# Optimization experiments

Hardware: AMD Instinct MI355X
Metric: run time of the kernel (lower is better)

Reference implementation:

```python
import jax, jax.numpy as jnp
import numpy as np

C, PE, L, HEADS = 256, 64, 6, 4
N_GRAPHS, S = 2048, 64            # uniform graphs of S nodes -> dense batch is a reshape
N = N_GRAPHS * S                  # 131072 nodes
E = N * 4                         # 524288 edges
BN_EPS = 1e-5


def _bn(h, g, b):
    # BatchNorm1d, training-mode statistics (biased variance), affine
    m = h.mean(0)
    v = h.var(0)
    return (h - m) / jnp.sqrt(v + BN_EPS) * g + b


def setup_inputs() -> dict:
    key = jax.random.key(0)
    ks = iter(jax.random.split(key, 64))
    def rn(shape, scale=0.05):
        return jax.random.normal(next(ks), shape, dtype=jnp.float32) * scale
    x = jax.random.randint(next(ks), (N, 1), 0, 28)
    pe = jax.random.normal(next(ks), (N, 20), dtype=jnp.float32)
    epg = E // N_GRAPHS
    base = (jnp.arange(E) // epg) * S          # edges stay within their graph
    src = base + jax.random.randint(next(ks), (E,), 0, S)
    dst = base + jax.random.randint(next(ks), (E,), 0, S)
    edge_index = jnp.stack([src, dst])
    edge_attr = jax.random.randint(next(ks), (E,), 0, 4)
    batch = jnp.arange(N) // S
    return dict(
        x=x, pe=pe, edge_index=edge_index, edge_attr=edge_attr, batch=batch,
        node_emb=rn((28, C - PE), 1.0), pe_lin_w=rn((20, PE)), pe_lin_b=jnp.zeros(PE),
        pe_norm_g=jnp.ones(20), pe_norm_b=jnp.zeros(20),
        edge_emb=rn((4, C), 1.0),
        conv_w1=rn((L, C, C)), conv_b1=jnp.zeros((L, C)),
        conv_w2=rn((L, C, C)), conv_b2=jnp.zeros((L, C)),
        attn_in_w=rn((L, C, 3 * C)), attn_in_b=jnp.zeros((L, 3 * C)),
        attn_out_w=rn((L, C, C)), attn_out_b=jnp.zeros((L, C)),
        bn1_g=jnp.ones((L, C)), bn1_b=jnp.zeros((L, C)),
        bn2_g=jnp.ones((L, C)), bn2_b=jnp.zeros((L, C)),
        bn3_g=jnp.ones((L, C)), bn3_b=jnp.zeros((L, C)),
        mlp_w1=rn((L, C, 2 * C)), mlp_b1=jnp.zeros((L, 2 * C)),
        mlp_w2=rn((L, 2 * C, C)), mlp_b2=jnp.zeros((L, C)),
        head_w1=rn((C, C // 2)), head_b1=jnp.zeros(C // 2),
        head_w2=rn((C // 2, C // 4)), head_b2=jnp.zeros(C // 4),
        head_w3=rn((C // 4, 1)), head_b3=jnp.zeros(1),
    )


def reference(x, pe, edge_index, edge_attr, batch, node_emb, pe_lin_w, pe_lin_b,
              pe_norm_g, pe_norm_b, edge_emb, conv_w1, conv_b1, conv_w2, conv_b2,
              attn_in_w, attn_in_b, attn_out_w, attn_out_b,
              bn1_g, bn1_b, bn2_g, bn2_b, bn3_g, bn3_b,
              mlp_w1, mlp_b1, mlp_w2, mlp_b2,
              head_w1, head_b1, head_w2, head_b2, head_w3, head_b3):
    x_pe = _bn(pe, pe_norm_g, pe_norm_b)
    h = jnp.concatenate([node_emb[x[:, 0]], x_pe @ pe_lin_w + pe_lin_b], axis=1)  # [N, C]
    ea = edge_emb[edge_attr]                                                      # [E, C]
    src, dst = edge_index[0], edge_index[1]
    d = C // HEADS
    scale = 1.0 / jnp.sqrt(jnp.float32(d))
    for l in range(L):
        # --- local GINEConv: nn((1+eps)*x_i + sum_j relu(x_j + e_ij)), eps=0 ---
        msg = jax.nn.relu(h[src] + ea)                          # gather + add + relu
        aggr = jax.ops.segment_sum(msg, dst, num_segments=N)    # scatter-add
        z = h + aggr
        hl = jax.nn.relu(z @ conv_w1[l] + conv_b1[l]) @ conv_w2[l] + conv_b2[l]
        hl = _bn(hl + h, bn1_g[l], bn1_b[l])                    # residual + norm1
        # --- global multihead attention on dense batch [G, S, C] ---
        hd = h.reshape(N_GRAPHS, S, C)
        qkv = hd @ attn_in_w[l] + attn_in_b[l]
        q, k, v = jnp.split(qkv, 3, axis=-1)
        q = q.reshape(N_GRAPHS, S, HEADS, d).transpose(0, 2, 1, 3)
        k = k.reshape(N_GRAPHS, S, HEADS, d).transpose(0, 2, 1, 3)
        v = v.reshape(N_GRAPHS, S, HEADS, d).transpose(0, 2, 1, 3)
        a = jax.nn.softmax(jnp.einsum('ghqd,ghkd->ghqk', q, k) * scale, axis=-1)
        o = jnp.einsum('ghqk,ghkd->ghqd', a, v).transpose(0, 2, 1, 3).reshape(N_GRAPHS, S, C)
        o = (o @ attn_out_w[l] + attn_out_b[l]).reshape(N, C)
        ha = _bn(o + h, bn2_g[l], bn2_b[l])                     # residual + norm2
        # --- combine + FFN ---
        out = hl + ha
        ff = jax.nn.relu(out @ mlp_w1[l] + mlp_b1[l]) @ mlp_w2[l] + mlp_b2[l]
        h = _bn(out + ff, bn3_g[l], bn3_b[l])                   # residual + norm3
    pooled = jax.ops.segment_sum(h, batch, num_segments=N_GRAPHS)  # global_add_pool -> [G, C]
    t = jax.nn.relu(pooled @ head_w1 + head_b1)
    t = jax.nn.relu(t @ head_w2 + head_b2)
    return t @ head_w3 + head_b3                                   # [G, 1]
```

## Files before the change

kernel.cpp:

```cpp
#include <hip/hip_runtime.h>

#define N_NODES 131072
#define N_EDGES 524288
#define CCH 256
#define N_GRAPHS_ 2048
#define SEQ 64
#define LAYERS 6

typedef unsigned short US;
typedef __attribute__((ext_vector_type(8))) short v8s;
typedef __attribute__((ext_vector_type(8))) unsigned short v8us;
typedef __attribute__((ext_vector_type(4))) float v4f;

__device__ __forceinline__ float b2f(US u) { return __uint_as_float(((unsigned)u) << 16); }
__device__ __forceinline__ US f2b(float f) {
    unsigned u = __float_as_uint(f);
    return (US)((u + 0x7fff + ((u >> 16) & 1)) >> 16);
}
__device__ __forceinline__ void gload16(const US* g, US* l) {
    __builtin_amdgcn_global_load_lds(
        (const __attribute__((address_space(1))) unsigned int*)g,
        (__attribute__((address_space(3))) unsigned int*)l, 16, 0, 0);
}

__device__ float g_stats[512];
__device__ float g_aff1[512];
__device__ float g_aff2[512];
__device__ float g_aff3[512];
__device__ float g_pe[40];
__device__ float g_peaff[40];
__device__ US    g_wt[6 * 655360];
__device__ int   g_csr[N_EDGES];
__device__ int   g_off[N_GRAPHS_ * 65];

__global__ __launch_bounds__(256) void wt_k(const float* __restrict__ cw1, const float* __restrict__ cw2,
                                            const float* __restrict__ aiw, const float* __restrict__ aow,
                                            const float* __restrict__ mw1, const float* __restrict__ mw2) {
    __shared__ float t[64][65];
    int b = blockIdx.x;
    int l = b / 160, r = b % 160;
    const float* src; int ldw, ldk, ctiles; size_t doff;
    if (r < 16)      { src = cw1 + (size_t)l * 65536;  ldw = 256; ldk = 256; ctiles = 4;  doff = 0;      }
    else if (r < 32) { src = cw2 + (size_t)l * 65536;  ldw = 256; ldk = 256; ctiles = 4;  doff = 65536;  r -= 16; }
    else if (r < 80) { src = aiw + (size_t)l * 196608; ldw = 768; ldk = 256; ctiles = 12; doff = 131072; r -= 32; }
    else if (r < 96) { src = aow + (size_t)l * 65536;  ldw = 256; ldk = 256; ctiles = 4;  doff = 327680; r -= 80; }
    else if (r < 128){ src = mw1 + (size_t)l * 131072; ldw = 512; ldk = 256; ctiles = 8;  doff = 393216; r -= 96; }
    else             { src = mw2 + (size_t)l * 131072; ldw = 256; ldk = 512; ctiles = 4;  doff = 524288; r -= 128; }
    int kt = r / ctiles, ct = r % ctiles;
    int k0 = kt * 64, c0 = ct * 64;
    US* dst = g_wt + (size_t)l * 655360 + doff;
    int tid = threadIdx.x;
    int rr = tid >> 4, c4 = (tid & 15) * 4;
    #pragma unroll
    for (int j = 0; j < 4; j++) {
        float4 v = *(const float4*)(src + (size_t)(k0 + rr + j * 16) * ldw + c0 + c4);
        t[rr + j * 16][c4 + 0] = v.x; t[rr + j * 16][c4 + 1] = v.y;
        t[rr + j * 16][c4 + 2] = v.z; t[rr + j * 16][c4 + 3] = v.w;
    }
    __syncthreads();
    #pragma unroll
    for (int j = 0; j < 4; j++) {
        int crow = rr + j * 16;
        ushort4 o;
        o.x = f2b(t[c4 + 0][crow]); o.y = f2b(t[c4 + 1][crow]);
        o.z = f2b(t[c4 + 2][crow]); o.w = f2b(t[c4 + 3][crow]);
        *(ushort4*)(dst + (size_t)(c0 + crow) * ldk + k0 + c4) = o;
    }
}

__global__ __launch_bounds__(256) void csr_k(const int* __restrict__ ei,
                                             const int* __restrict__ attr) {
    __shared__ int deg[64], off[65];
    int g = blockIdx.x, tid = threadIdx.x;
    if (tid < 64) deg[tid] = 0;
    __syncthreads();
    int e = g * 256 + tid;
    int d = ei[N_EDGES + e] - g * 64;
    int slot = atomicAdd(&deg[d], 1);
    __syncthreads();
    if (tid == 0) {
        off[0] = 0;
        for (int i = 0; i < 64; i++) off[i + 1] = off[i] + deg[i];
    }
    __syncthreads();
    g_csr[g * 256 + off[d] + slot] = (ei[e] - g * 64) | (attr[e] << 6);
    if (tid < 65) g_off[g * 65 + tid] = off[tid];
}

__global__ __launch_bounds__(256) void pe_part_k(const float* __restrict__ pe) {
    __shared__ float red[240], red2[240];
    int b = blockIdx.x, tid = threadIdx.x;
    float s = 0.f, s2 = 0.f;
    if (tid < 240) {
        int ch = tid % 20, sub = tid / 20;
        size_t r0 = (size_t)b * 512;
        for (int r = sub; r < 512; r += 12) {
            float v = pe[(r0 + r) * 20 + ch];
            s += v; s2 += v * v;
        }
        red[tid] = s; red2[tid] = s2;
    }
    __syncthreads();
    if (tid < 20) {
        float ts = 0.f, ts2 = 0.f;
        #pragma unroll
        for (int sub = 0; sub < 12; sub++) { ts += red[sub * 20 + tid]; ts2 += red2[sub * 20 + tid]; }
        atomicAdd(&g_pe[tid], ts);
        atomicAdd(&g_pe[20 + tid], ts2);
    }
}

__global__ __launch_bounds__(64) void pe_fin_k(const float* __restrict__ g,
                                               const float* __restrict__ b) {
    int t = threadIdx.x;
    if (t < 20) {
        float mean = g_pe[t] / (float)N_NODES;
        float var  = g_pe[20 + t] / (float)N_NODES - mean * mean;
        float a = g[t] * rsqrtf(var + 1e-5f);
        g_peaff[t] = a;
        g_peaff[20 + t] = b[t] - mean * a;
        g_pe[t] = 0.f;
        g_pe[20 + t] = 0.f;
    }
}

__global__ __launch_bounds__(256) void embed_k(const int* __restrict__ x,
                                               const float* __restrict__ pe,
                                               const float* __restrict__ node_emb,
                                               const float* __restrict__ plw,
                                               const float* __restrict__ plb,
                                               US* __restrict__ h) {
    int n = blockIdx.x;
    int tid = threadIdx.x;
    int xi = x[n];
    float v;
    if (tid < 192) {
        v = node_emb[xi * 192 + tid];
    } else {
        int j = tid - 192;
        float s = plb[j];
        #pragma unroll
        for (int k = 0; k < 20; k++) {
            float p = pe[(size_t)n * 20 + k] * g_peaff[k] + g_peaff[20 + k];
            s += p * plw[k * 64 + j];
        }
        v = s;
    }
    h[(size_t)n * CCH + tid] = f2b(v);
}

__global__ __launch_bounds__(256) void aggr_z_k(const US* __restrict__ h,
                                                const float* __restrict__ eemb,
                                                US* __restrict__ z) {
    __shared__ US ht[64 * 264];
    __shared__ float em[4 * 260];
    __shared__ int off[65], ce[256];
    int g = blockIdx.x, tid = threadIdx.x;
    for (int v = tid; v < 2048; v += 256) {
        int row = v >> 5, seg = (v & 31) * 8;
        *(v8us*)&ht[row * 264 + seg] = *(const v8us*)(h + (size_t)(g * 64 + row) * 256 + seg);
    }
    for (int i = tid; i < 1024; i += 256)
        em[(i >> 8) * 260 + (i & 255)] = eemb[(i >> 8) * 256 + (i & 255)];
    ce[tid] = g_csr[g * 256 + tid];
    if (tid < 65) off[tid] = g_off[g * 65 + tid];
    __syncthreads();

    int dst = tid >> 2, cq = (tid & 3) * 4;
    float acc[64];
    #pragma unroll
    for (int i = 0; i < 64; i++) acc[i] = 0.f;
    int e1 = off[dst + 1];
    for (int e = off[dst]; e < e1; e++) {
        int val = ce[e];
        int src = val & 63, a = (val >> 6) & 3;
        #pragma unroll
        for (int i = 0; i < 16; i++) {
            int c = cq + i * 16;
            ushort4 hv = *(ushort4*)&ht[src * 264 + c];
            float4 ev = *(float4*)&em[a * 260 + c];
            acc[i * 4 + 0] += fmaxf(b2f(hv.x) + ev.x, 0.f);
            acc[i * 4 + 1] += fmaxf(b2f(hv.y) + ev.y, 0.f);
            acc[i * 4 + 2] += fmaxf(b2f(hv.z) + ev.z, 0.f);
            acc[i * 4 + 3] += fmaxf(b2f(hv.w) + ev.w, 0.f);
        }
    }
    US* zp = z + (size_t)(g * 64 + dst) * 256;
    #pragma unroll
    for (int i = 0; i < 16; i++) {
        int c = cq + i * 16;
        ushort4 hv = *(ushort4*)&ht[dst * 264 + c];
        ushort4 o;
        o.x = f2b(b2f(hv.x) + acc[i * 4 + 0]);
        o.y = f2b(b2f(hv.y) + acc[i * 4 + 1]);
        o.z = f2b(b2f(hv.z) + acc[i * 4 + 2]);
        o.w = f2b(b2f(hv.w) + acc[i * 4 + 3]);
        *(ushort4*)(zp + c) = o;
    }
}

template<int NG, bool STATS>
__global__ __launch_bounds__(256, 4) void gemm_mfma_k(const US* __restrict__ A,
                                                      size_t woff, int ldk,
                                                      int w0, int w1, int w2, int w3,
                                                      const float* __restrict__ bias,
                                                      const US* __restrict__ res,
                                                      US* __restrict__ Y, int mode) {
    const US* __restrict__ Wt = g_wt + woff;
    __shared__ __align__(16) char smem[8192 + 2 * NG * 4096];
    US* As0 = (US*)smem;
    US* As1 = As0 + 2048;
    US* Bs0 = (US*)(smem + 8192);
    US* Bs1 = Bs0 + NG * 2048;
    float* Es = (float*)smem;
    const int NW = NG * 64 + 4;

    int tid = threadIdx.x;
    int bid = blockIdx.x;
    int swz = (bid & 7) * ((int)gridDim.x >> 3) + (bid >> 3);
    size_t row0 = (size_t)swz * 64;
    int w = tid >> 6, l = tid & 63;
    int li = l & 15, hi = l >> 4;
    int sl = hi ^ ((li >> 1) & 3);
    int sr = l >> 2, ss = l & 3;

    int a_off = (w * 16 + li) * 32 + sl * 8;

    v4f acc[NG * 4];
    #pragma unroll
    for (int t = 0; t < NG * 4; t++) acc[t] = (v4f){0.f, 0.f, 0.f, 0.f};

    int ar = w * 16 + sr;
    int akg = (ss ^ ((ar >> 1) & 3)) * 8;
    const US* asrc = A + (row0 + ar) * 256 + akg;

    auto stage = [&](int kc, US* Asb, US* Bsb) {
        int k0 = kc * 32;
        gload16(asrc + k0, Asb + w * 512);
        #pragma unroll
        for (int j = 0; j < NG; j++) {
            int cu = (j * 4 + w) * 16 + sr;
            int grp = cu >> 6;
            int wb = (grp == 0) ? w0 : (grp == 1) ? w1 : (grp == 2) ? w2 : w3;
            int kg = (ss ^ ((cu >> 1) & 3)) * 8;
            gload16(Wt + (size_t)(wb + (cu & 63)) * ldk + k0 + kg,
                    Bsb + (j * 4 + w) * 512);
        }
    };

    stage(0, As0, Bs0);
    __syncthreads();
    for (int kc = 0; kc < 8; kc++) {
        US* Asc = (kc & 1) ? As1 : As0;
        US* Bsc = (kc & 1) ? Bs1 : Bs0;
        if (kc < 7) stage(kc + 1, (kc & 1) ? As0 : As1, (kc & 1) ? Bs0 : Bs1);
        v8s a0 = *(v8s*)(Asc + a_off);
        #pragma unroll
        for (int t = 0; t < NG * 4; t++) {
            v8s bf = *(v8s*)(Bsc + (t * 16 + li) * 32 + sl * 8);
            acc[t] = __builtin_amdgcn_mfma_f32_16x16x32_bf16(a0, bf, acc[t], 0, 0, 0);
        }
        __syncthreads();
    }

    int er_f = tid >> 3;
    int lcb = (tid & 7) * 8;
    float csum = 0.f, csum2 = 0.f;
    #pragma unroll
    for (int p = 0; p < 2; p++) {
        if ((w >> 1) == p) {
            int er0 = (w & 1) * 16 + hi * 4;
            #pragma unroll
            for (int t = 0; t < NG * 4; t++) {
                int grp = t >> 2;
                int wb = (grp == 0) ? w0 : (grp == 1) ? w1 : (grp == 2) ? w2 : w3;
                float bv = bias ? bias[wb + (t & 3) * 16 + li] : 0.f;
                #pragma unroll
                for (int r = 0; r < 4; r++) {
                    float v = acc[t][r] + bv;
                    if (mode == 1) v = fmaxf(v, 0.f);
                    Es[(er0 + r) * NW + t * 16 + li] = v;
                }
            }
        }
        __syncthreads();
        size_t gr = row0 + p * 32 + er_f;
        #pragma unroll
        for (int s = 0; s < NG; s++) {
            int c = s * 64 + lcb;
            float vs[8];
            #pragma unroll
            for (int j = 0; j < 8; j++) vs[j] = Es[er_f * NW + c + j];
            if (mode == 2) {
                v8us rv = *(const v8us*)(res + gr * 256 + c);
                #pragma unroll
                for (int j = 0; j < 8; j++) vs[j] += b2f(rv[j]);
            }
            v8us yv;
            #pragma unroll
            for (int j = 0; j < 8; j++) yv[j] = f2b(vs[j]);
            *(v8us*)(Y + gr * 256 + c) = yv;
            if constexpr (STATS) {
                #pragma unroll
                for (int j = 0; j < 8; j++) Es[er_f * NW + c + j] = vs[j];
            }
        }
        if constexpr (STATS) {
            __syncthreads();
            if (tid < NG * 64) {
                float s1 = 0.f, s2 = 0.f;
                #pragma unroll 8
                for (int r2 = 0; r2 < 32; r2++) {
                    float vv = Es[r2 * NW + tid];
                    s1 += vv; s2 += vv * vv;
                }
                csum += s1; csum2 += s2;
            }
        }
        __syncthreads();
    }
    if constexpr (STATS) {
        if (tid < NG * 64) {
            atomicAdd(&g_stats[tid], csum);
            atomicAdd(&g_stats[CCH + tid], csum2);
        }
    }
}

template<int NH>
__global__ __launch_bounds__(256, 2) void mlp_fused_k(const US* __restrict__ A,
                                                      size_t woff1, const float* __restrict__ bias1,
                                                      size_t woff2, int ldk2,
                                                      const float* __restrict__ bias2,
                                                      const US* __restrict__ res,
                                                      US* __restrict__ Y) {
    const US* __restrict__ W1t = g_wt + woff1;
    const US* __restrict__ W2t = g_wt + woff2;
    __shared__ __align__(16) char smem[73728];
    US* As0 = (US*)smem;
    US* As1 = (US*)(smem + 4096);
    US* Bs0 = (US*)(smem + 8192);
    US* Bs1 = (US*)(smem + 24576);
    float* Es = (float*)smem;
    US* Ts = (US*)(smem + 40960);

    int tid = threadIdx.x;
    int bid = blockIdx.x;
    int swz = (bid & 7) * ((int)gridDim.x >> 3) + (bid >> 3);
    size_t row0 = (size_t)swz * 64;
    int w = tid >> 6, l = tid & 63;
    int li = l & 15, hi = l >> 4;
    int sl = hi ^ ((li >> 1) & 3);
    int sr = l >> 2, ss = l & 3;

    int a_off = (w * 16 + li) * 32 + sl * 8;

    v4f accY[16];
    #pragma unroll
    for (int t = 0; t < 16; t++) accY[t] = (v4f){0.f, 0.f, 0.f, 0.f};

    int ar = w * 16 + sr;
    int akg = (ss ^ ((ar >> 1) & 3)) * 8;
    const US* asrc = A + (row0 + ar) * 256 + akg;

    #pragma unroll
    for (int q = 0; q < NH; q++) {
        v4f accT[16];
        #pragma unroll
        for (int t = 0; t < 16; t++) accT[t] = (v4f){0.f, 0.f, 0.f, 0.f};

        auto stageA = [&](int kc, US* Asb, US* Bsb) {
            int k0 = kc * 32;
            gload16(asrc + k0, Asb + w * 512);
            #pragma unroll
            for (int j = 0; j < 4; j++) {
                int cu = (j * 4 + w) * 16 + sr;
                int kg = (ss ^ ((cu >> 1) & 3)) * 8;
                gload16(W1t + (size_t)(q * 256 + cu) * 256 + k0 + kg,
                        Bsb + (j * 4 + w) * 512);
            }
        };
        stageA(0, As0, Bs0);
        __syncthreads();
        for (int kc = 0; kc < 8; kc++) {
            US* Asc = (kc & 1) ? As1 : As0;
            US* Bsc = (kc & 1) ? Bs1 : Bs0;
            if (kc < 7) stageA(kc + 1, (kc & 1) ? As0 : As1, (kc & 1) ? Bs0 : Bs1);
            v8s a0 = *(v8s*)(Asc + a_off);
            #pragma unroll
            for (int t = 0; t < 16; t++) {
                v8s bf = *(v8s*)(Bsc + (t * 16 + li) * 32 + sl * 8);
                accT[t] = __builtin_amdgcn_mfma_f32_16x16x32_bf16(a0, bf, accT[t], 0, 0, 0);
            }
            __syncthreads();
        }
        #pragma unroll
        for (int p = 0; p < 2; p++) {
            if ((w >> 1) == p) {
                int er0 = (w & 1) * 16 + hi * 4;
                #pragma unroll
                for (int t = 0; t < 16; t++) {
                    float bv = bias1[q * 256 + t * 16 + li];
                    #pragma unroll
                    for (int r = 0; r < 4; r++)
                        Es[(er0 + r) * 260 + t * 16 + li] = fmaxf(accT[t][r] + bv, 0.f);
                }
            }
            __syncthreads();
            {
                int er = tid >> 3, lcb = (tid & 7) * 8;
                int rowL = p * 32 + er;
                int rsw = (rowL >> 1) & 3;
                #pragma unroll
                for (int s = 0; s < 4; s++) {
                    int col = s * 64 + lcb;
                    v8us tv;
                    #pragma unroll
                    for (int j = 0; j < 8; j++) tv[j] = f2b(Es[er * 260 + col + j]);
                    int chunk = col >> 5, slot = ((col >> 3) & 3) ^ rsw;
                    *(v8us*)&Ts[chunk * 2048 + rowL * 32 + slot * 8] = tv;
                }
            }
            __syncthreads();
        }
        auto stageB = [&](int kc, US* Bsb) {
            int k0 = q * 256 + kc * 32;
            #pragma unroll
            for (int j = 0; j < 4; j++) {
                int cu = (j * 4 + w) * 16 + sr;
                int kg = (ss ^ ((cu >> 1) & 3)) * 8;
                gload16(W2t + (size_t)cu * ldk2 + k0 + kg, Bsb + (j * 4 + w) * 512);
            }
        };
        stageB(0, Bs0);
        __syncthreads();
        for (int kc = 0; kc < 8; kc++) {
            US* Bsc = (kc & 1) ? Bs1 : Bs0;
            if (kc < 7) stageB(kc + 1, (kc & 1) ? Bs0 : Bs1);
            v8s a0 = *(v8s*)(Ts + kc * 2048 + a_off);
            #pragma unroll
            for (int t = 0; t < 16; t++) {
                v8s bf = *(v8s*)(Bsc + (t * 16 + li) * 32 + sl * 8);
                accY[t] = __builtin_amdgcn_mfma_f32_16x16x32_bf16(a0, bf, accY[t], 0, 0, 0);
            }
            __syncthreads();
        }
    }

    int er_f = tid >> 3;
    int lcb = (tid & 7) * 8;
    float csum = 0.f, csum2 = 0.f;
    #pragma unroll
    for (int p = 0; p < 2; p++) {
        if ((w >> 1) == p) {
            int er0 = (w & 1) * 16 + hi * 4;
            #pragma unroll
            for (int t = 0; t < 16; t++) {
                float bv = bias2[t * 16 + li];
                #pragma unroll
                for (int r = 0; r < 4; r++)
                    Es[(er0 + r) * 260 + t * 16 + li] = accY[t][r] + bv;
            }
        }
        __syncthreads();
        size_t gr = row0 + p * 32 + er_f;
        #pragma unroll
        for (int s = 0; s < 4; s++) {
            int c = s * 64 + lcb;
            float vs[8];
            #pragma unroll
            for (int j = 0; j < 8; j++) vs[j] = Es[er_f * 260 + c + j];
            v8us rv = *(const v8us*)(res + gr * 256 + c);
            #pragma unroll
            for (int j = 0; j < 8; j++) vs[j] += b2f(rv[j]);
            v8us yv;
            #pragma unroll
            for (int j = 0; j < 8; j++) yv[j] = f2b(vs[j]);
            *(v8us*)(Y + gr * 256 + c) = yv;
            #pragma unroll
            for (int j = 0; j < 8; j++) Es[er_f * 260 + c + j] = vs[j];
        }
        __syncthreads();
        {
            float s1 = 0.f, s2 = 0.f;
            #pragma unroll 8
            for (int r2 = 0; r2 < 32; r2++) {
                float vv = Es[r2 * 260 + tid];
                s1 += vv; s2 += vv * vv;
            }
            csum += s1; csum2 += s2;
        }
        __syncthreads();
    }
    atomicAdd(&g_stats[tid], csum);
    atomicAdd(&g_stats[CCH + tid], csum2);
}

__global__ __launch_bounds__(64) void attn_k(const US* __restrict__ qkv,
                                             US* __restrict__ o) {
    __shared__ __align__(16) US Ps[64 * 72];
    __shared__ __align__(16) US Vt[64 * 72];
    int g = blockIdx.x, l = threadIdx.x;
    int li = l & 15, hi8 = (l >> 4) * 8, hi4 = (l >> 4) * 4;
    const US* base = qkv + (size_t)g * 64 * 256;

    {
        v8us vv[8];
        #pragma unroll
        for (int jv = 0; jv < 8; jv++)
            vv[jv] = *(const v8us*)(base + l * 256 + 128 + jv * 8);
        #pragma unroll
        for (int jv = 0; jv < 8; jv++)
            #pragma unroll
            for (int e = 0; e < 8; e++)
                Vt[(jv * 8 + e) * 72 + l] = vv[jv][e];
    }

    v8s Qf[4][2], Kf[4][2];
    #pragma unroll
    for (int t = 0; t < 4; t++)
        #pragma unroll
        for (int ds = 0; ds < 2; ds++) {
            Qf[t][ds] = *(const v8s*)(base + (t * 16 + li) * 256 + ds * 32 + hi8);
            Kf[t][ds] = *(const v8s*)(base + (t * 16 + li) * 256 + 64 + ds * 32 + hi8);
        }

    v4f S[4][4];
    #pragma unroll
    for (int qt = 0; qt < 4; qt++)
        #pragma unroll
        for (int kt = 0; kt < 4; kt++) {
            v4f a = (v4f){0.f, 0.f, 0.f, 0.f};
            a = __builtin_amdgcn_mfma_f32_16x16x32_bf16(Qf[qt][0], Kf[kt][0], a, 0, 0, 0);
            a = __builtin_amdgcn_mfma_f32_16x16x32_bf16(Qf[qt][1], Kf[kt][1], a, 0, 0, 0);
            S[qt][kt] = a;
        }

    #pragma unroll
    for (int qt = 0; qt < 4; qt++)
        #pragma unroll
        for (int r = 0; r < 4; r++) {
            float mx = -1e30f;
            #pragma unroll
            for (int kt = 0; kt < 4; kt++) {
                S[qt][kt][r] *= 0.125f;
                mx = fmaxf(mx, S[qt][kt][r]);
            }
            mx = fmaxf(mx, __shfl_xor(mx, 1));
            mx = fmaxf(mx, __shfl_xor(mx, 2));
            mx = fmaxf(mx, __shfl_xor(mx, 4));
            mx = fmaxf(mx, __shfl_xor(mx, 8));
            float sum = 0.f;
            #pragma unroll
            for (int kt = 0; kt < 4; kt++) {
                float e = __expf(S[qt][kt][r] - mx);
                S[qt][kt][r] = e;
                sum += e;
            }
            sum += __shfl_xor(sum, 1);
            sum += __shfl_xor(sum, 2);
            sum += __shfl_xor(sum, 4);
            sum += __shfl_xor(sum, 8);
            float inv = 1.f / sum;
            #pragma unroll
            for (int kt = 0; kt < 4; kt++)
                Ps[(qt * 16 + hi4 + r) * 72 + kt * 16 + li] = f2b(S[qt][kt][r] * inv);
        }

    v4f O[4][4];
    #pragma unroll
    for (int qt = 0; qt < 4; qt++)
        #pragma unroll
        for (int jt = 0; jt < 4; jt++) O[qt][jt] = (v4f){0.f, 0.f, 0.f, 0.f};
    #pragma unroll
    for (int ks = 0; ks < 2; ks++) {
        v8s Pf[4], Vf[4];
        #pragma unroll
        for (int qt = 0; qt < 4; qt++)
            Pf[qt] = *(v8s*)&Ps[(qt * 16 + li) * 72 + ks * 32 + hi8];
        #pragma unroll
        for (int jt = 0; jt < 4; jt++)
            Vf[jt] = *(v8s*)&Vt[(jt * 16 + li) * 72 + ks * 32 + hi8];
        #pragma unroll
        for (int qt = 0; qt < 4; qt++)
            #pragma unroll
            for (int jt = 0; jt < 4; jt++)
                O[qt][jt] = __builtin_amdgcn_mfma_f32_16x16x32_bf16(Pf[qt], Vf[jt], O[qt][jt], 0, 0, 0);
    }

    #pragma unroll
    for (int qt = 0; qt < 4; qt++)
        #pragma unroll
        for (int jt = 0; jt < 4; jt++)
            #pragma unroll
            for (int r = 0; r < 4; r++)
                Ps[(qt * 16 + hi4 + r) * 72 + jt * 16 + li] = f2b(O[qt][jt][r]);
    US* ob = o + (size_t)(g * 64 + l) * 256;
    #pragma unroll
    for (int jv = 0; jv < 8; jv++)
        *(v8us*)(ob + jv * 8) = *(v8us*)&Ps[l * 72 + jv * 8];
}

__global__ __launch_bounds__(256) void affine_k(const float* __restrict__ g,
                                                const float* __restrict__ b, int sel) {
    int c = threadIdx.x;
    float mean = g_stats[c] / (float)N_NODES;
    float var  = g_stats[CCH + c] / (float)N_NODES - mean * mean;
    float a = g[c] * rsqrtf(var + 1e-5f);
    float* dst = (sel == 0) ? g_aff1 : (sel == 1) ? g_aff2 : g_aff3;
    dst[c] = a;
    dst[CCH + c] = b[c] - mean * a;
    g_stats[c] = 0.f;
    g_stats[CCH + c] = 0.f;
}

__global__ __launch_bounds__(256) void combine_k(const US* __restrict__ y1,
                                                 const US* __restrict__ y2,
                                                 US* __restrict__ out) {
    size_t idx = (size_t)blockIdx.x * 256 + threadIdx.x;
    size_t stride = (size_t)gridDim.x * 256;
    for (; idx < (size_t)N_NODES * CCH / 8; idx += stride) {
        size_t i = idx * 8;
        int c = (int)(i & 255);
        v8us a = *(const v8us*)(y1 + i);
        v8us b = *(const v8us*)(y2 + i);
        v8us o;
        #pragma unroll
        for (int j = 0; j < 8; j++) {
            float v = b2f(a[j]) * g_aff1[c + j] + g_aff1[CCH + c + j] +
                      b2f(b[j]) * g_aff2[c + j] + g_aff2[CCH + c + j];
            o[j] = f2b(v);
        }
        *(v8us*)(out + i) = o;
    }
}

__global__ __launch_bounds__(256) void apply_k(US* __restrict__ h) {
    size_t idx = (size_t)blockIdx.x * 256 + threadIdx.x;
    size_t stride = (size_t)gridDim.x * 256;
    for (; idx < (size_t)N_NODES * CCH / 8; idx += stride) {
        size_t i = idx * 8;
        int c = (int)(i & 255);
        v8us a = *(const v8us*)(h + i);
        v8us o;
        #pragma unroll
        for (int j = 0; j < 8; j++)
            o[j] = f2b(b2f(a[j]) * g_aff3[c + j] + g_aff3[CCH + c + j]);
        *(v8us*)(h + i) = o;
    }
}

__global__ __launch_bounds__(256) void pool_k(const US* __restrict__ h,
                                              float* __restrict__ pooled) {
    int g = blockIdx.x, c = threadIdx.x;
    float s = 0.f;
    for (int ss = 0; ss < SEQ; ss++) s += b2f(h[((size_t)g * SEQ + ss) * CCH + c]);
    pooled[(size_t)g * CCH + c] = s;
}

__global__ __launch_bounds__(128) void head_k(const float* __restrict__ pooled,
                                              const float* __restrict__ w1, const float* __restrict__ b1,
                                              const float* __restrict__ w2, const float* __restrict__ b2,
                                              const float* __restrict__ w3, const float* __restrict__ b3,
                                              float* __restrict__ outp) {
    __shared__ float p[256], t1[128], t2[64];
    int g = blockIdx.x, tid = threadIdx.x;
    p[tid] = pooled[(size_t)g * CCH + tid];
    p[tid + 128] = pooled[(size_t)g * CCH + 128 + tid];
    __syncthreads();
    float s = b1[tid];
    for (int k = 0; k < 256; k++) s += p[k] * w1[k * 128 + tid];
    t1[tid] = fmaxf(s, 0.f);
    __syncthreads();
    if (tid < 64) {
        float s2 = b2[tid];
        for (int k = 0; k < 128; k++) s2 += t1[k] * w2[k * 64 + tid];
        t2[tid] = fmaxf(s2, 0.f);
    }
    __syncthreads();
    if (tid == 0) {
        float s3 = b3[0];
        for (int k = 0; k < 64; k++) s3 += t2[k] * w3[k];
        outp[g] = s3;
    }
}

extern "C" void kernel_launch(void* const* d_in, const int* in_sizes, int n_in,
                              void* d_out, int out_size, void* d_ws, size_t ws_size,
                              hipStream_t stream) {
    const int*   x         = (const int*)  d_in[0];
    const float* pe        = (const float*)d_in[1];
    const int*   ei        = (const int*)  d_in[2];
    const int*   eattr     = (const int*)  d_in[3];
    const float* node_emb  = (const float*)d_in[5];
    const float* pe_lin_w  = (const float*)d_in[6];
    const float* pe_lin_b  = (const float*)d_in[7];
    const float* pe_norm_g = (const float*)d_in[8];
    const float* pe_norm_b = (const float*)d_in[9];
    const float* edge_emb  = (const float*)d_in[10];
    const float* conv_w1   = (const float*)d_in[11];
    const float* conv_b1   = (const float*)d_in[12];
    const float* conv_w2   = (const float*)d_in[13];
    const float* conv_b2   = (const float*)d_in[14];
    const float* attn_in_w = (const float*)d_in[15];
    const float* attn_in_b = (const float*)d_in[16];
    const float* attn_out_w= (const float*)d_in[17];
    const float* attn_out_b= (const float*)d_in[18];
    const float* bn1_g     = (const float*)d_in[19];
    const float* bn1_b     = (const float*)d_in[20];
    const float* bn2_g     = (const float*)d_in[21];
    const float* bn2_b     = (const float*)d_in[22];
    const float* bn3_g     = (const float*)d_in[23];
    const float* bn3_b     = (const float*)d_in[24];
    const float* mlp_w1    = (const float*)d_in[25];
    const float* mlp_b1    = (const float*)d_in[26];
    const float* mlp_w2    = (const float*)d_in[27];
    const float* mlp_b2    = (const float*)d_in[28];
    const float* head_w1   = (const float*)d_in[29];
    const float* head_b1   = (const float*)d_in[30];
    const float* head_w2   = (const float*)d_in[31];
    const float* head_b2   = (const float*)d_in[32];
    const float* head_w3   = (const float*)d_in[33];
    const float* head_b3   = (const float*)d_in[34];
    (void)in_sizes; (void)n_in; (void)out_size; (void)ws_size;

    char* ws = (char*)d_ws;
    US* h = (US*)(ws);
    US* A = (US*)(ws + 67108864ULL);
    US* B = (US*)(ws + 134217728ULL);
    US* C = (US*)(ws + 201326592ULL);
    float* pooled = (float*)(ws + 67108864ULL);

    wt_k<<<960, 256, 0, stream>>>(conv_w1, conv_w2, attn_in_w, attn_out_w, mlp_w1, mlp_w2);
    csr_k<<<N_GRAPHS_, 256, 0, stream>>>(ei, eattr);
    pe_part_k<<<256, 256, 0, stream>>>(pe);
    pe_fin_k<<<1, 64, 0, stream>>>(pe_norm_g, pe_norm_b);
    embed_k<<<N_NODES, 256, 0, stream>>>(x, pe, node_emb, pe_lin_w, pe_lin_b, h);

    for (int l = 0; l < LAYERS; l++) {
        size_t wl = (size_t)l * 655360;

        aggr_z_k<<<N_GRAPHS_, 256, 0, stream>>>(h, edge_emb, A);
        mlp_fused_k<1><<<2048, 256, 0, stream>>>(A, wl, conv_b1 + l * 256,
                                                 wl + 65536, 256, conv_b2 + l * 256,
                                                 h, C);
        affine_k<<<1, 256, 0, stream>>>(bn1_g + l * 256, bn1_b + l * 256, 0);

        for (int hh = 0; hh < 4; hh++) {
            gemm_mfma_k<3, false><<<2048, 256, 0, stream>>>(h, wl + 131072, 256,
                                                            hh * 64, 256 + hh * 64, 512 + hh * 64, 0,
                                                            attn_in_b + l * 768, nullptr, A, 0);
            attn_k<<<N_GRAPHS_, 64, 0, stream>>>(A, B + hh * 64);
        }
        gemm_mfma_k<4, true><<<2048, 256, 0, stream>>>(B, wl + 327680, 256, 0, 64, 128, 192,
                                                       attn_out_b + l * 256, h, h, 2);
        affine_k<<<1, 256, 0, stream>>>(bn2_g + l * 256, bn2_b + l * 256, 1);

        combine_k<<<2048, 256, 0, stream>>>(C, h, A);
        mlp_fused_k<2><<<2048, 256, 0, stream>>>(A, wl + 393216, mlp_b1 + l * 512,
                                                 wl + 524288, 512, mlp_b2 + l * 256,
                                                 A, h);
        affine_k<<<1, 256, 0, stream>>>(bn3_g + l * 256, bn3_b + l * 256, 2);
        apply_k<<<2048, 256, 0, stream>>>(h);
    }

    pool_k<<<N_GRAPHS_, 256, 0, stream>>>(h, pooled);
    head_k<<<N_GRAPHS_, 128, 0, stream>>>(pooled, head_w1, head_b1, head_w2, head_b2,
                                          head_w3, head_b3, (float*)d_out);
}
```

Measured before the change: 5.097 ms.

## Fuse BN combine into FFN GEMM and defer BN3 apply into next consumers

Removes the standalone combine kernel by computing the BN1/BN2 affine sum inside the FFN GEMM's A-tile staging and residual epilogue. It also removes the standalone BN3 apply kernel: the next layer's aggregation applies the affine while loading h and writes the normalized h back, and pool_k folds the final affine into the pooled sum. This saves two full elementwise passes over the 64MB activation per layer. In exchange, the FFN A staging switches from direct-to-LDS global loads to register loads with extra math, and that work is repeated for each hidden half.

```diff
diff --git a/kernel.cpp b/kernel.cpp
--- a/kernel.cpp
+++ b/kernel.cpp
@@ -149,16 +149,25 @@
     h[(size_t)n * CCH + tid] = f2b(v);
 }
 
-__global__ __launch_bounds__(256) void aggr_z_k(const US* __restrict__ h,
+__global__ __launch_bounds__(256) void aggr_z_k(US* __restrict__ h,
                                                 const float* __restrict__ eemb,
-                                                US* __restrict__ z) {
+                                                US* __restrict__ z, int useAff) {
     __shared__ US ht[64 * 264];
     __shared__ float em[4 * 260];
     __shared__ int off[65], ce[256];
     int g = blockIdx.x, tid = threadIdx.x;
     for (int v = tid; v < 2048; v += 256) {
         int row = v >> 5, seg = (v & 31) * 8;
-        *(v8us*)&ht[row * 264 + seg] = *(const v8us*)(h + (size_t)(g * 64 + row) * 256 + seg);
+        v8us hv = *(const v8us*)(h + (size_t)(g * 64 + row) * 256 + seg);
+        if (useAff) {
+            v8us o;
+            #pragma unroll
+            for (int j = 0; j < 8; j++)
+                o[j] = f2b(b2f(hv[j]) * g_aff3[seg + j] + g_aff3[CCH + seg + j]);
+            hv = o;
+            *(v8us*)(h + (size_t)(g * 64 + row) * 256 + seg) = hv;
+        }
+        *(v8us*)&ht[row * 264 + seg] = hv;
     }
     for (int i = tid; i < 1024; i += 256)
         em[(i >> 8) * 260 + (i & 255)] = eemb[(i >> 8) * 256 + (i & 255)];
@@ -327,8 +336,9 @@
     }
 }
 
-template<int NH>
+template<int NH, bool COMB>
 __global__ __launch_bounds__(256, 2) void mlp_fused_k(const US* __restrict__ A,
+                                                      const US* __restrict__ H2,
                                                       size_t woff1, const float* __restrict__ bias1,
                                                       size_t woff2, int ldk2,
                                                       const float* __restrict__ bias2,
@@ -362,6 +372,7 @@
     int ar = w * 16 + sr;
     int akg = (ss ^ ((ar >> 1) & 3)) * 8;
     const US* asrc = A + (row0 + ar) * 256 + akg;
+    const US* hsrc = COMB ? (H2 + (row0 + ar) * 256 + akg) : nullptr;
 
     #pragma unroll
     for (int q = 0; q < NH; q++) {
@@ -371,7 +382,21 @@
 
         auto stageA = [&](int kc, US* Asb, US* Bsb) {
             int k0 = kc * 32;
-            gload16(asrc + k0, Asb + w * 512);
+            if constexpr (COMB) {
+                int cidx = k0 + akg;
+                v8us cv = *(const v8us*)(asrc + k0);
+                v8us hv = *(const v8us*)(hsrc + k0);
+                v8us t;
+                #pragma unroll
+                for (int j = 0; j < 8; j++) {
+                    float v = b2f(cv[j]) * g_aff1[cidx + j] + g_aff1[CCH + cidx + j] +
+                              b2f(hv[j]) * g_aff2[cidx + j] + g_aff2[CCH + cidx + j];
+                    t[j] = f2b(v);
+                }
+                *(v8us*)&Asb[w * 512 + l * 8] = t;
+            } else {
+                gload16(asrc + k0, Asb + w * 512);
+            }
             #pragma unroll
             for (int j = 0; j < 4; j++) {
                 int cu = (j * 4 + w) * 16 + sr;
@@ -470,9 +495,20 @@
             float vs[8];
             #pragma unroll
             for (int j = 0; j < 8; j++) vs[j] = Es[er_f * 260 + c + j];
-            v8us rv = *(const v8us*)(res + gr * 256 + c);
-            #pragma unroll
-            for (int j = 0; j < 8; j++) vs[j] += b2f(rv[j]);
+            if constexpr (COMB) {
+                v8us c8 = *(const v8us*)(A + gr * 256 + c);
+                v8us h8 = *(const v8us*)(H2 + gr * 256 + c);
+                #pragma unroll
+                for (int j = 0; j < 8; j++) {
+                    float cb = b2f(c8[j]) * g_aff1[c + j] + g_aff1[CCH + c + j] +
+                               b2f(h8[j]) * g_aff2[c + j] + g_aff2[CCH + c + j];
+                    vs[j] += b2f(f2b(cb));
+                }
+            } else {
+                v8us rv = *(const v8us*)(res + gr * 256 + c);
+                #pragma unroll
+                for (int j = 0; j < 8; j++) vs[j] += b2f(rv[j]);
+            }
             v8us yv;
             #pragma unroll
             for (int j = 0; j < 8; j++) yv[j] = f2b(vs[j]);
@@ -614,48 +650,12 @@
     g_stats[CCH + c] = 0.f;
 }
 
-__global__ __launch_bounds__(256) void combine_k(const US* __restrict__ y1,
-                                                 const US* __restrict__ y2,
-                                                 US* __restrict__ out) {
-    size_t idx = (size_t)blockIdx.x * 256 + threadIdx.x;
-    size_t stride = (size_t)gridDim.x * 256;
-    for (; idx < (size_t)N_NODES * CCH / 8; idx += stride) {
-        size_t i = idx * 8;
-        int c = (int)(i & 255);
-        v8us a = *(const v8us*)(y1 + i);
-        v8us b = *(const v8us*)(y2 + i);
-        v8us o;
-        #pragma unroll
-        for (int j = 0; j < 8; j++) {
-            float v = b2f(a[j]) * g_aff1[c + j] + g_aff1[CCH + c + j] +
-                      b2f(b[j]) * g_aff2[c + j] + g_aff2[CCH + c + j];
-            o[j] = f2b(v);
-        }
-        *(v8us*)(out + i) = o;
-    }
-}
-
-__global__ __launch_bounds__(256) void apply_k(US* __restrict__ h) {
-    size_t idx = (size_t)blockIdx.x * 256 + threadIdx.x;
-    size_t stride = (size_t)gridDim.x * 256;
-    for (; idx < (size_t)N_NODES * CCH / 8; idx += stride) {
-        size_t i = idx * 8;
-        int c = (int)(i & 255);
-        v8us a = *(const v8us*)(h + i);
-        v8us o;
-        #pragma unroll
-        for (int j = 0; j < 8; j++)
-            o[j] = f2b(b2f(a[j]) * g_aff3[c + j] + g_aff3[CCH + c + j]);
-        *(v8us*)(h + i) = o;
-    }
-}
-
 __global__ __launch_bounds__(256) void pool_k(const US* __restrict__ h,
                                               float* __restrict__ pooled) {
     int g = blockIdx.x, c = threadIdx.x;
     float s = 0.f;
     for (int ss = 0; ss < SEQ; ss++) s += b2f(h[((size_t)g * SEQ + ss) * CCH + c]);
-    pooled[(size_t)g * CCH + c] = s;
+    pooled[(size_t)g * CCH + c] = g_aff3[c] * s + 64.f * g_aff3[CCH + c];
 }
 
 __global__ __launch_bounds__(128) void head_k(const float* __restrict__ pooled,
@@ -740,10 +740,10 @@
     for (int l = 0; l < LAYERS; l++) {
         size_t wl = (size_t)l * 655360;
 
-        aggr_z_k<<<N_GRAPHS_, 256, 0, stream>>>(h, edge_emb, A);
-        mlp_fused_k<1><<<2048, 256, 0, stream>>>(A, wl, conv_b1 + l * 256,
-                                                 wl + 65536, 256, conv_b2 + l * 256,
-                                                 h, C);
+        aggr_z_k<<<N_GRAPHS_, 256, 0, stream>>>(h, edge_emb, A, l == 0 ? 0 : 1);
+        mlp_fused_k<1, false><<<2048, 256, 0, stream>>>(A, nullptr, wl, conv_b1 + l * 256,
+                                                        wl + 65536, 256, conv_b2 + l * 256,
+                                                        h, C);
         affine_k<<<1, 256, 0, stream>>>(bn1_g + l * 256, bn1_b + l * 256, 0);
 
         for (int hh = 0; hh < 4; hh++) {
@@ -756,12 +756,10 @@
                                                        attn_out_b + l * 256, h, h, 2);
         affine_k<<<1, 256, 0, stream>>>(bn2_g + l * 256, bn2_b + l * 256, 1);
 
-        combine_k<<<2048, 256, 0, stream>>>(C, h, A);
-        mlp_fused_k<2><<<2048, 256, 0, stream>>>(A, wl + 393216, mlp_b1 + l * 512,
-                                                 wl + 524288, 512, mlp_b2 + l * 256,
-                                                 A, h);
+        mlp_fused_k<2, true><<<2048, 256, 0, stream>>>(C, h, wl + 393216, mlp_b1 + l * 512,
+                                                       wl + 524288, 512, mlp_b2 + l * 256,
+                                                       nullptr, h);
         affine_k<<<1, 256, 0, stream>>>(bn3_g + l * 256, bn3_b + l * 256, 2);
-        apply_k<<<2048, 256, 0, stream>>>(h);
     }
 
     pool_k<<<N_GRAPHS_, 256, 0, stream>>>(h, pooled);
```

Result: slower. 5.235 ms (+2.7%).

## Batch QKV projection across heads and fold final BN into pooling

Applied to the files above, without the earlier changes.

Replaces the per-head loop of four QKV gemm plus attention launches with three full-width gemms producing Q, K and V buffers and a single attention launch over a 2D grid of graphs by heads, writing output in place into the Q buffer. The last layer's BN3 apply is folded into pool_k as an affine on the sum, and the apply pass is moved to the start of each subsequent layer. Buffer usage is reshuffled (attention residual output goes to B, aggregation to C). This cuts launch count and redundant reads of h per head, at the cost of an extra full-size intermediate buffer and added syncs in attn_k.

```diff
diff --git a/kernel.cpp b/kernel.cpp
--- a/kernel.cpp
+++ b/kernel.cpp
@@ -149,6 +149,21 @@
     h[(size_t)n * CCH + tid] = f2b(v);
 }
 
+__global__ __launch_bounds__(256) void apply_k(US* __restrict__ h) {
+    size_t idx = (size_t)blockIdx.x * 256 + threadIdx.x;
+    size_t stride = (size_t)gridDim.x * 256;
+    for (; idx < (size_t)N_NODES * CCH / 8; idx += stride) {
+        size_t i = idx * 8;
+        int c = (int)(i & 255);
+        v8us a = *(const v8us*)(h + i);
+        v8us o;
+        #pragma unroll
+        for (int j = 0; j < 8; j++)
+            o[j] = f2b(b2f(a[j]) * g_aff3[c + j] + g_aff3[CCH + c + j]);
+        *(v8us*)(h + i) = o;
+    }
+}
+
 __global__ __launch_bounds__(256) void aggr_z_k(const US* __restrict__ h,
                                                 const float* __restrict__ eemb,
                                                 US* __restrict__ z) {
@@ -496,19 +511,21 @@
     atomicAdd(&g_stats[CCH + tid], csum2);
 }
 
-__global__ __launch_bounds__(64) void attn_k(const US* __restrict__ qkv,
-                                             US* __restrict__ o) {
+__global__ __launch_bounds__(64) void attn_k(US* __restrict__ qb,
+                                             const US* __restrict__ kb,
+                                             const US* __restrict__ vb) {
     __shared__ __align__(16) US Ps[64 * 72];
     __shared__ __align__(16) US Vt[64 * 72];
     int g = blockIdx.x, l = threadIdx.x;
+    int coff = blockIdx.y * 64;
     int li = l & 15, hi8 = (l >> 4) * 8, hi4 = (l >> 4) * 4;
-    const US* base = qkv + (size_t)g * 64 * 256;
+    size_t rb = (size_t)g * 64 * 256;
 
     {
         v8us vv[8];
         #pragma unroll
         for (int jv = 0; jv < 8; jv++)
-            vv[jv] = *(const v8us*)(base + l * 256 + 128 + jv * 8);
+            vv[jv] = *(const v8us*)(vb + rb + l * 256 + coff + jv * 8);
         #pragma unroll
         for (int jv = 0; jv < 8; jv++)
             #pragma unroll
@@ -521,8 +538,8 @@
     for (int t = 0; t < 4; t++)
         #pragma unroll
         for (int ds = 0; ds < 2; ds++) {
-            Qf[t][ds] = *(const v8s*)(base + (t * 16 + li) * 256 + ds * 32 + hi8);
-            Kf[t][ds] = *(const v8s*)(base + (t * 16 + li) * 256 + 64 + ds * 32 + hi8);
+            Qf[t][ds] = *(const v8s*)(qb + rb + (t * 16 + li) * 256 + coff + ds * 32 + hi8);
+            Kf[t][ds] = *(const v8s*)(kb + rb + (t * 16 + li) * 256 + coff + ds * 32 + hi8);
         }
 
     v4f S[4][4];
@@ -588,6 +605,7 @@
                 O[qt][jt] = __builtin_amdgcn_mfma_f32_16x16x32_bf16(Pf[qt], Vf[jt], O[qt][jt], 0, 0, 0);
     }
 
+    __syncthreads();
     #pragma unroll
     for (int qt = 0; qt < 4; qt++)
         #pragma unroll
@@ -595,7 +613,8 @@
             #pragma unroll
             for (int r = 0; r < 4; r++)
                 Ps[(qt * 16 + hi4 + r) * 72 + jt * 16 + li] = f2b(O[qt][jt][r]);
-    US* ob = o + (size_t)(g * 64 + l) * 256;
+    __syncthreads();
+    US* ob = qb + rb + l * 256 + coff;
     #pragma unroll
     for (int jv = 0; jv < 8; jv++)
         *(v8us*)(ob + jv * 8) = *(v8us*)&Ps[l * 72 + jv * 8];
@@ -635,27 +654,12 @@
     }
 }
 
-__global__ __launch_bounds__(256) void apply_k(US* __restrict__ h) {
-    size_t idx = (size_t)blockIdx.x * 256 + threadIdx.x;
-    size_t stride = (size_t)gridDim.x * 256;
-    for (; idx < (size_t)N_NODES * CCH / 8; idx += stride) {
-        size_t i = idx * 8;
-        int c = (int)(i & 255);
-        v8us a = *(const v8us*)(h + i);
-        v8us o;
-        #pragma unroll
-        for (int j = 0; j < 8; j++)
-            o[j] = f2b(b2f(a[j]) * g_aff3[c + j] + g_aff3[CCH + c + j]);
-        *(v8us*)(h + i) = o;
-    }
-}
-
 __global__ __launch_bounds__(256) void pool_k(const US* __restrict__ h,
                                               float* __restrict__ pooled) {
     int g = blockIdx.x, c = threadIdx.x;
     float s = 0.f;
     for (int ss = 0; ss < SEQ; ss++) s += b2f(h[((size_t)g * SEQ + ss) * CCH + c]);
-    pooled[(size_t)g * CCH + c] = s;
+    pooled[(size_t)g * CCH + c] = g_aff3[c] * s + 64.f * g_aff3[CCH + c];
 }
 
 __global__ __launch_bounds__(128) void head_k(const float* __restrict__ pooled,
@@ -740,28 +744,30 @@
     for (int l = 0; l < LAYERS; l++) {
         size_t wl = (size_t)l * 655360;
 
-        aggr_z_k<<<N_GRAPHS_, 256, 0, stream>>>(h, edge_emb, A);
-        mlp_fused_k<1><<<2048, 256, 0, stream>>>(A, wl, conv_b1 + l * 256,
+        if (l > 0) apply_k<<<2048, 256, 0, stream>>>(h);
+
+        gemm_mfma_k<4, false><<<2048, 256, 0, stream>>>(h, wl + 131072, 256, 0, 64, 128, 192,
+                                                        attn_in_b + l * 768, nullptr, A, 0);
+        gemm_mfma_k<4, false><<<2048, 256, 0, stream>>>(h, wl + 131072, 256, 256, 320, 384, 448,
+                                                        attn_in_b + l * 768, nullptr, B, 0);
+        gemm_mfma_k<4, false><<<2048, 256, 0, stream>>>(h, wl + 131072, 256, 512, 576, 640, 704,
+                                                        attn_in_b + l * 768, nullptr, C, 0);
+        attn_k<<<dim3(N_GRAPHS_, 4), 64, 0, stream>>>(A, B, C);
+        gemm_mfma_k<4, true><<<2048, 256, 0, stream>>>(A, wl + 327680, 256, 0, 64, 128, 192,
+                                                       attn_out_b + l * 256, h, B, 2);
+        affine_k<<<1, 256, 0, stream>>>(bn2_g + l * 256, bn2_b + l * 256, 1);
+
+        aggr_z_k<<<N_GRAPHS_, 256, 0, stream>>>(h, edge_emb, C);
+        mlp_fused_k<1><<<2048, 256, 0, stream>>>(C, wl, conv_b1 + l * 256,
                                                  wl + 65536, 256, conv_b2 + l * 256,
                                                  h, C);
         affine_k<<<1, 256, 0, stream>>>(bn1_g + l * 256, bn1_b + l * 256, 0);
 
-        for (int hh = 0; hh < 4; hh++) {
-            gemm_mfma_k<3, false><<<2048, 256, 0, stream>>>(h, wl + 131072, 256,
-                                                            hh * 64, 256 + hh * 64, 512 + hh * 64, 0,
-                                                            attn_in_b + l * 768, nullptr, A, 0);
-            attn_k<<<N_GRAPHS_, 64, 0, stream>>>(A, B + hh * 64);
-        }
-        gemm_mfma_k<4, true><<<2048, 256, 0, stream>>>(B, wl + 327680, 256, 0, 64, 128, 192,
-                                                       attn_out_b + l * 256, h, h, 2);
-        affine_k<<<1, 256, 0, stream>>>(bn2_g + l * 256, bn2_b + l * 256, 1);
-
-        combine_k<<<2048, 256, 0, stream>>>(C, h, A);
+        combine_k<<<2048, 256, 0, stream>>>(C, B, A);
         mlp_fused_k<2><<<2048, 256, 0, stream>>>(A, wl + 393216, mlp_b1 + l * 512,
                                                  wl + 524288, 512, mlp_b2 + l * 256,
                                                  A, h);
         affine_k<<<1, 256, 0, stream>>>(bn3_g + l * 256, bn3_b + l * 256, 2);
-        apply_k<<<2048, 256, 0, stream>>>(h);
     }
 
     pool_k<<<N_GRAPHS_, 256, 0, stream>>>(h, pooled);
```

Result: no change. 5.023 ms (median of 2 runs) (-1.4%).
